# Kernel optimization log

Hardware: AMD Instinct MI355X
Metric: run time of the kernel (lower is better)

## Reference

```python
import jax, jax.numpy as jnp
import numpy as np

N_NODES = 100000
N_EDGES = 1600000
DIM = 3
HID = 128
BN_EPS = 1e-5


def _bn(x, g, b):
    # BatchNorm1d, training-mode batch statistics (biased variance, like torch)
    m = jnp.mean(x, axis=0)
    v = jnp.var(x, axis=0)
    return (x - m) * jax.lax.rsqrt(v + BN_EPS) * g + b


def _gin_mlp(h, w1, b1, g1, be1, w2, b2, g2, be2, w3, b3):
    # Linear -> BN -> ReLU -> (Dropout: identity in eval) -> Linear -> BN -> ReLU -> Linear
    h = jax.nn.relu(_bn(h @ w1 + b1, g1, be1))
    h = jax.nn.relu(_bn(h @ w2 + b2, g2, be2))
    return h @ w3 + b3


def _gin_conv(x, src, dst, eps, mlp_params):
    # GINConv: mlp((1+eps)*x_i + sum_{j->i} x_j); scatter-add over edge targets
    agg = jax.ops.segment_sum(x[src], dst, num_segments=N_NODES)
    return _gin_mlp((1.0 + eps) * x + agg, *mlp_params)


def setup_inputs() -> dict:
    key = jax.random.key(0)
    ks = jax.random.split(key, 32)

    def w(k, shape, scale=0.05):
        return jax.random.normal(k, shape, dtype=jnp.float32) * scale

    inp = {}
    inp["coords"] = jax.random.normal(ks[0], (N_NODES, DIM), dtype=jnp.float32)
    inp["edge_index"] = jax.random.randint(ks[1], (2, N_EDGES), 0, N_NODES, dtype=jnp.int32)

    # GIN layer 0 MLP (dim -> hid -> hid -> hid)
    inp["g0_w1"] = w(ks[2], (DIM, HID)); inp["g0_b1"] = jnp.zeros((HID,), jnp.float32)
    inp["g0_g1"] = jnp.ones((HID,), jnp.float32); inp["g0_be1"] = jnp.zeros((HID,), jnp.float32)
    inp["g0_w2"] = w(ks[3], (HID, HID)); inp["g0_b2"] = jnp.zeros((HID,), jnp.float32)
    inp["g0_g2"] = jnp.ones((HID,), jnp.float32); inp["g0_be2"] = jnp.zeros((HID,), jnp.float32)
    inp["g0_w3"] = w(ks[4], (HID, HID)); inp["g0_b3"] = jnp.zeros((HID,), jnp.float32)
    inp["eps0"] = jnp.zeros((), jnp.float32)
    inp["bn0_g"] = jnp.ones((HID,), jnp.float32); inp["bn0_b"] = jnp.zeros((HID,), jnp.float32)

    # GIN layer 1 MLP (hid -> hid -> hid -> hid)
    inp["g1_w1"] = w(ks[5], (HID, HID)); inp["g1_b1"] = jnp.zeros((HID,), jnp.float32)
    inp["g1_g1"] = jnp.ones((HID,), jnp.float32); inp["g1_be1"] = jnp.zeros((HID,), jnp.float32)
    inp["g1_w2"] = w(ks[6], (HID, HID)); inp["g1_b2"] = jnp.zeros((HID,), jnp.float32)
    inp["g1_g2"] = jnp.ones((HID,), jnp.float32); inp["g1_be2"] = jnp.zeros((HID,), jnp.float32)
    inp["g1_w3"] = w(ks[7], (HID, HID)); inp["g1_b3"] = jnp.zeros((HID,), jnp.float32)
    inp["eps1"] = jnp.zeros((), jnp.float32)
    inp["bn1_g"] = jnp.ones((HID,), jnp.float32); inp["bn1_b"] = jnp.zeros((HID,), jnp.float32)

    # decoder MLP: (2*hid+1) -> hid -> hid//2 -> 1, sigmoid
    inp["d_w1"] = w(ks[8], (2 * HID + 1, HID)); inp["d_b1"] = jnp.zeros((HID,), jnp.float32)
    inp["d_g"] = jnp.ones((HID,), jnp.float32); inp["d_be"] = jnp.zeros((HID,), jnp.float32)
    inp["d_w2"] = w(ks[9], (HID, HID // 2)); inp["d_b2"] = jnp.zeros((HID // 2,), jnp.float32)
    inp["d_w3"] = w(ks[10], (HID // 2, 1)); inp["d_b3"] = jnp.zeros((1,), jnp.float32)
    return inp


def reference(coords, edge_index,
              g0_w1, g0_b1, g0_g1, g0_be1, g0_w2, g0_b2, g0_g2, g0_be2, g0_w3, g0_b3, eps0, bn0_g, bn0_b,
              g1_w1, g1_b1, g1_g1, g1_be1, g1_w2, g1_b2, g1_g2, g1_be2, g1_w3, g1_b3, eps1, bn1_g, bn1_b,
              d_w1, d_b1, d_g, d_be, d_w2, d_b2, d_w3, d_b3):
    node_0 = edge_index[0]
    node_1 = edge_index[1]

    mlp0 = (g0_w1, g0_b1, g0_g1, g0_be1, g0_w2, g0_b2, g0_g2, g0_be2, g0_w3, g0_b3)
    mlp1 = (g1_w1, g1_b1, g1_g1, g1_be1, g1_w2, g1_b2, g1_g2, g1_be2, g1_w3, g1_b3)

    x = _gin_conv(coords, node_0, node_1, eps0, mlp0)
    x = jax.nn.relu(_bn(x, bn0_g, bn0_b))
    x = _gin_conv(x, node_0, node_1, eps1, mlp1)
    x = jax.nn.relu(_bn(x, bn1_g, bn1_b))

    # edge_l_cntr branch: per-edge contour-length feature + endpoint concat
    l = jnp.linalg.norm(coords[node_1] - coords[node_0], axis=1, keepdims=True)  # [E,1]
    h = jnp.concatenate([x[node_0], x[node_1], l], axis=-1)  # [E, 2*hid+1]

    h = jax.nn.relu(_bn(h @ d_w1 + d_b1, d_g, d_be))
    h = jax.nn.relu(h @ d_w2 + d_b2)
    out = jax.nn.sigmoid((h @ d_w3 + d_b3).squeeze(-1))  # [E]
    return out
```

## Files before the change

### kernel.cpp

```cpp
#include <hip/hip_runtime.h>
#include <hip/hip_bf16.h>
#include <math.h>


typedef __attribute__((ext_vector_type(8))) __bf16 bf16x8;
typedef __attribute__((ext_vector_type(4))) float f32x4;

__device__ __forceinline__ unsigned int pack_bf16(float a, float b) {
    unsigned short ua = __builtin_bit_cast(unsigned short, __float2bfloat16(a));
    unsigned short ub = __builtin_bit_cast(unsigned short, __float2bfloat16(b));
    return (unsigned int)ua | ((unsigned int)ub << 16);
}
__device__ __forceinline__ float bflo(unsigned int u) {
    return __builtin_bit_cast(float, u << 16);
}
__device__ __forceinline__ float bfhi(unsigned int u) {
    return __builtin_bit_cast(float, u & 0xffff0000u);
}
__device__ __forceinline__ unsigned short bf16r(float a) {
    return __builtin_bit_cast(unsigned short, __float2bfloat16(a));
}


__global__ void hist_dst(const int* __restrict__ edst, int* __restrict__ cursor, int E) {
    int e = blockIdx.x * 256 + threadIdx.x;
    if (e < E) atomicAdd(&cursor[edst[e]], 1);
}

__global__ __launch_bounds__(1024) void scan_deg(const int* deg, int* rowoff, int* cursor, int N) {
    __shared__ int sums[1024];
    const int t = threadIdx.x;
    const int chunk = (N + 1023) >> 10;
    int lo = t * chunk, hi = lo + chunk;
    if (lo > N) lo = N;
    if (hi > N) hi = N;
    int s = 0;
    for (int i = lo; i < hi; ++i) s += deg[i];
    sums[t] = s;
    __syncthreads();
    for (int off = 1; off < 1024; off <<= 1) {
        int add = (t >= off) ? sums[t - off] : 0;
        __syncthreads();
        sums[t] += add;
        __syncthreads();
    }
    int run = sums[t] - s;
    for (int i = lo; i < hi; ++i) {
        int d = deg[i];
        rowoff[i] = run;
        cursor[i] = run;
        run += d;
    }
    if (t == 1023) rowoff[N] = sums[1023];
}

__global__ void fill_csr(const int* __restrict__ esrc, const int* __restrict__ edst,
                         const float* __restrict__ coords,
                         int* cursor, int* __restrict__ perm, int* __restrict__ dperm,
                         int* __restrict__ eperm, float* __restrict__ lperm, int E) {
    int e = blockIdx.x * 256 + threadIdx.x;
    if (e >= E) return;
    int s0 = esrc[e], d0 = edst[e];
    int pos = atomicAdd(&cursor[d0], 1);
    perm[pos] = s0;
    dperm[pos] = d0;
    eperm[pos] = e;
    float dx = coords[d0*3+0] - coords[s0*3+0];
    float dy = coords[d0*3+1] - coords[s0*3+1];
    float dz = coords[d0*3+2] - coords[s0*3+2];
    lperm[pos] = sqrtf(dx*dx + dy*dy + dz*dz);
}


__global__ void gather_coords(const float* __restrict__ coords,
                              const int* __restrict__ rowoff, const int* __restrict__ perm,
                              float* __restrict__ agg0, int N) {
    int i = blockIdx.x * 256 + threadIdx.x;
    if (i >= N) return;
    float ax = 0.f, ay = 0.f, az = 0.f;
    int b = rowoff[i], t = rowoff[i+1];
    for (int j = b; j < t; ++j) {
        int p = perm[j];
        ax += coords[p*3+0];
        ay += coords[p*3+1];
        az += coords[p*3+2];
    }
    agg0[i*3+0] = ax; agg0[i*3+1] = ay; agg0[i*3+2] = az;
}

__global__ __launch_bounds__(256) void gather_combine_bn(const unsigned short* __restrict__ x,
                                                         const int* __restrict__ rowoff,
                                                         const int* __restrict__ perm,
                                                         const float* __restrict__ st,
                                                         const float* __restrict__ g,
                                                         const float* __restrict__ be,
                                                         float invN,
                                                         const float* __restrict__ eps,
                                                         unsigned short* __restrict__ y, int N) {
    int node = blockIdx.x * 4 + (threadIdx.x >> 6);
    int lane = threadIdx.x & 63;
    if (node >= N) return;
    float ep = 1.f + *eps;
    int c0 = lane*2, c1 = c0 + 1;
    float m0 = st[c0]*invN, m1 = st[c1]*invN;
    float v0 = fmaxf(st[128+c0]*invN - m0*m0, 0.f);
    float v1 = fmaxf(st[128+c1]*invN - m1*m1, 0.f);
    float a0 = g[c0]*rsqrtf(v0 + 1e-5f), a1 = g[c1]*rsqrtf(v1 + 1e-5f);
    float sx = a0, sy = a1;
    float hx = be[c0] - m0*a0, hy = be[c1] - m1*a1;
    const unsigned int* x2 = (const unsigned int*)x;
    int b = rowoff[node], t = rowoff[node+1];
    float accx = 0.f, accy = 0.f;
    int j = b;
    for (; j + 2 <= t; j += 2) {
        unsigned int u0 = x2[(size_t)perm[j]*64 + lane];
        unsigned int u1 = x2[(size_t)perm[j+1]*64 + lane];
        accx += fmaxf(fmaf(bflo(u0), sx, hx), 0.f) + fmaxf(fmaf(bflo(u1), sx, hx), 0.f);
        accy += fmaxf(fmaf(bfhi(u0), sy, hy), 0.f) + fmaxf(fmaf(bfhi(u1), sy, hy), 0.f);
    }
    if (j < t) {
        unsigned int u = x2[(size_t)perm[j]*64 + lane];
        accx += fmaxf(fmaf(bflo(u), sx, hx), 0.f);
        accy += fmaxf(fmaf(bfhi(u), sy, hy), 0.f);
    }
    unsigned int uo = x2[(size_t)node*64 + lane];
    accx = fmaf(ep, fmaxf(fmaf(bflo(uo), sx, hx), 0.f), accx);
    accy = fmaf(ep, fmaxf(fmaf(bfhi(uo), sy, hy), 0.f), accy);
    ((unsigned int*)y)[(size_t)node*64 + lane] = pack_bf16(accx, accy);
}


__global__ __launch_bounds__(256) void lin0(const float* __restrict__ coords,
                                            const float* __restrict__ agg0,
                                            const float* __restrict__ W1,
                                            const float* __restrict__ b1,
                                            const float* __restrict__ eps0,
                                            unsigned short* __restrict__ t1,
                                            float* __restrict__ stats, int nrows) {
    int col = threadIdx.x & 127, half = threadIdx.x >> 7;
    float w0 = W1[col], w1 = W1[128+col], w2 = W1[256+col], bb = b1[col];
    float ep = 1.f + *eps0;
    float s = 0.f, q = 0.f;
    int r0 = blockIdx.x * 64;
    for (int i = 0; i < 32; ++i) {
        int row = r0 + half + 2*i;
        if (row < nrows) {
            float h0 = fmaf(ep, coords[row*3+0], agg0[row*3+0]);
            float h1 = fmaf(ep, coords[row*3+1], agg0[row*3+1]);
            float h2 = fmaf(ep, coords[row*3+2], agg0[row*3+2]);
            float v = fmaf(h0, w0, fmaf(h1, w1, fmaf(h2, w2, bb)));
            t1[row*128+col] = bf16r(v);
            s += v; q += v*v;
        }
    }
    __shared__ float red[512];
    red[half*128+col] = s;
    red[256 + half*128+col] = q;
    __syncthreads();
    if (threadIdx.x < 128) {
        atomicAdd(&stats[col],       red[col] + red[128+col]);
        atomicAdd(&stats[128+col],   red[256+col] + red[384+col]);
    }
}

__global__ void prep_w2(const float* __restrict__ W2, unsigned short* __restrict__ w2t) {
    int i = blockIdx.x * 256 + threadIdx.x;
    if (i >= 128*64) return;
    int k = i >> 6, c = i & 63;
    w2t[c*128 + k] = bf16r(W2[i]);
}

__global__ void prep_wT(const float* __restrict__ w0, const float* __restrict__ w1,
                        const float* __restrict__ w2, const float* __restrict__ w3,
                        const float* __restrict__ w4, const float* __restrict__ w5,
                        const float* __restrict__ w6, unsigned short* __restrict__ dst) {
    int m = blockIdx.y;
    const float* src = (m==0)?w0:(m==1)?w1:(m==2)?w2:(m==3)?w3:(m==4)?w4:(m==5)?w5:w6;
    int i = blockIdx.x * 256 + threadIdx.x;
    int k = i >> 7, c = i & 127;
    dst[m*16384 + c*128 + k] = bf16r(src[i]);
}

template<bool IN_BN, bool STATS>
__global__ __launch_bounds__(256) void gemm_mfma(const unsigned short* __restrict__ A,
                                                 const unsigned short* __restrict__ wT,
                                                 const float* __restrict__ bias,
                                                 const float* __restrict__ inst,
                                                 const float* __restrict__ bng,
                                                 const float* __restrict__ bnb,
                                                 float invCnt,
                                                 unsigned short* __restrict__ Cb,
                                                 float* __restrict__ stats, int nrows) {
    __shared__ int4 sAi[1024];
    __shared__ int4 sBi[2048];
    __shared__ float sred[2][4][128];
    char* sA = (char*)sAi;
    char* sB = (char*)sBi;
    float* sSC = &sred[0][0][0];
    float* sSH = &sred[0][1][0];
    const int tid = threadIdx.x;
    const int tile0 = blockIdx.x * 64;

    if (IN_BN) {
        if (tid < 128) {
            float m = inst[tid] * invCnt;
            float v = fmaxf(inst[128+tid] * invCnt - m*m, 0.f);
            float a = bng[tid] * rsqrtf(v + 1e-5f);
            sSC[tid] = a;
            sSH[tid] = bnb[tid] - m*a;
        }
        __syncthreads();
    }

    {
        const int4* src = (const int4*)wT;
        #pragma unroll
        for (int ii = 0; ii < 8; ++ii) {
            int s = tid + 256*ii;
            int col = s >> 4, k16 = s & 15;
            int byte = ((col << 8) + (k16 << 4)) ^ ((col & 7) << 4);
            *(int4*)(sB + byte) = src[s];
        }
    }
    {
        const int4* A4 = (const int4*)A;
        #pragma unroll
        for (int ii = 0; ii < 4; ++ii) {
            int s = tid + 256*ii;
            int r = s >> 4, k16 = s & 15;
            int row = tile0 + r;
            int4 raw = make_int4(0,0,0,0);
            if (row < nrows) raw = A4[(size_t)row*16 + k16];
            if (IN_BN) {
                float4 sa = ((const float4*)sSC)[k16*2];
                float4 sb = ((const float4*)sSC)[k16*2+1];
                float4 ha = ((const float4*)sSH)[k16*2];
                float4 hb = ((const float4*)sSH)[k16*2+1];
                unsigned int ux = raw.x, uy = raw.y, uz = raw.z, uw = raw.w;
                float e0 = fmaxf(fmaf(bflo(ux), sa.x, ha.x), 0.f);
                float e1 = fmaxf(fmaf(bfhi(ux), sa.y, ha.y), 0.f);
                float e2 = fmaxf(fmaf(bflo(uy), sa.z, ha.z), 0.f);
                float e3 = fmaxf(fmaf(bfhi(uy), sa.w, ha.w), 0.f);
                float e4 = fmaxf(fmaf(bflo(uz), sb.x, hb.x), 0.f);
                float e5 = fmaxf(fmaf(bfhi(uz), sb.y, hb.y), 0.f);
                float e6 = fmaxf(fmaf(bflo(uw), sb.z, hb.z), 0.f);
                float e7 = fmaxf(fmaf(bfhi(uw), sb.w, hb.w), 0.f);
                raw.x = (int)pack_bf16(e0, e1);
                raw.y = (int)pack_bf16(e2, e3);
                raw.z = (int)pack_bf16(e4, e5);
                raw.w = (int)pack_bf16(e6, e7);
            }
            int byte = ((r << 8) + (k16 << 4)) ^ ((r & 7) << 4);
            *(int4*)(sA + byte) = raw;
        }
    }
    __syncthreads();

    const int l = tid & 63;
    const int w = tid >> 6;
    const int arow = (w << 4) + (l & 15);
    const int kbase = (l >> 4) << 3;
    f32x4 accv[8];
    #pragma unroll
    for (int c = 0; c < 8; ++c) accv[c] = (f32x4){0.f, 0.f, 0.f, 0.f};

    #pragma unroll
    for (int t = 0; t < 4; ++t) {
        int k0 = t*32 + kbase;
        int abyte = ((arow << 8) + (k0 << 1)) ^ ((arow & 7) << 4);
        bf16x8 af = __builtin_bit_cast(bf16x8, *(const int4*)(sA + abyte));
        #pragma unroll
        for (int c = 0; c < 8; ++c) {
            int bcol = (c << 4) + (l & 15);
            int bbyte = ((bcol << 8) + (k0 << 1)) ^ ((bcol & 7) << 4);
            bf16x8 bf = __builtin_bit_cast(bf16x8, *(const int4*)(sB + bbyte));
            accv[c] = __builtin_amdgcn_mfma_f32_16x16x32_bf16(af, bf, accv[c], 0, 0, 0);
        }
    }

    const int rj = (l >> 4) << 2;
    float lsum[8], lsq[8];
    #pragma unroll
    for (int c = 0; c < 8; ++c) {
        int col = (c << 4) + (l & 15);
        float bv = bias ? bias[col] : 0.f;
        f32x4 a = accv[c];
        float s = 0.f, q = 0.f;
        #pragma unroll
        for (int j = 0; j < 4; ++j) {
            int row = tile0 + (w << 4) + rj + j;
            float o = a[j] + bv;
            if (row < nrows) {
                Cb[(size_t)row*128 + col] = bf16r(o);
                if (STATS) { s += o; q += o*o; }
            }
        }
        lsum[c] = s; lsq[c] = q;
    }
    if (STATS) {
        #pragma unroll
        for (int c = 0; c < 8; ++c) {
            lsum[c] += __shfl_xor(lsum[c], 16, 64);
            lsum[c] += __shfl_xor(lsum[c], 32, 64);
            lsq[c]  += __shfl_xor(lsq[c], 16, 64);
            lsq[c]  += __shfl_xor(lsq[c], 32, 64);
        }
        __syncthreads();
        if ((l >> 4) == 0) {
            #pragma unroll
            for (int c = 0; c < 8; ++c) {
                int col = (c << 4) + l;
                sred[0][w][col] = lsum[c];
                sred[1][w][col] = lsq[c];
            }
        }
        __syncthreads();
        if (tid < 128) {
            float s = sred[0][0][tid] + sred[0][1][tid] + sred[0][2][tid] + sred[0][3][tid];
            float q = sred[1][0][tid] + sred[1][1][tid] + sred[1][2][tid] + sred[1][3][tid];
            atomicAdd(&stats[tid], s);
            atomicAdd(&stats[128 + tid], q);
        }
    }
}

__global__ __launch_bounds__(256) void csr_stats(const unsigned short* __restrict__ ya,
                                                 const unsigned short* __restrict__ yb,
                                                 const int* __restrict__ rowoff,
                                                 const int* __restrict__ perm,
                                                 const float* __restrict__ lperm,
                                                 const float* __restrict__ wl,
                                                 const float* __restrict__ b1,
                                                 float* __restrict__ stats, int N, int nspan) {
    int w = blockIdx.x * 4 + (threadIdx.x >> 6);
    int lane = threadIdx.x & 63;
    const unsigned int* ya2 = (const unsigned int*)ya;
    const unsigned int* yb2 = (const unsigned int*)yb;
    float2 wl2 = ((const float2*)wl)[lane];
    float2 b12 = ((const float2*)b1)[lane];
    float2 s = make_float2(0.f, 0.f), q = make_float2(0.f, 0.f);
    int i0 = w * nspan;
    int i1 = i0 + nspan; if (i1 > N) i1 = N;
    for (int i = i0; i < i1; ++i) {
        unsigned int ub = yb2[(size_t)i*64 + lane];
        float ybx = bflo(ub), yby = bfhi(ub);
        int b = rowoff[i], t = rowoff[i+1];
        for (int j = b; j < t; ++j) {
            int p = perm[j];
            float lv = lperm[j];
            unsigned int ua = ya2[(size_t)p*64 + lane];
            float zx = bflo(ua) + ybx + fmaf(lv, wl2.x, b12.x);
            float zy = bfhi(ua) + yby + fmaf(lv, wl2.y, b12.y);
            s.x += zx; s.y += zy;
            q.x += zx*zx; q.y += zy*zy;
        }
    }
    __shared__ float red[1024];
    int wv = threadIdx.x >> 6;
    red[wv*128 + lane*2]       = s.x;
    red[wv*128 + lane*2 + 1]   = s.y;
    red[512 + wv*128 + lane*2]     = q.x;
    red[512 + wv*128 + lane*2 + 1] = q.y;
    __syncthreads();
    if (threadIdx.x < 128) {
        int c = threadIdx.x;
        float ss = red[c] + red[128+c] + red[256+c] + red[384+c];
        float qq = red[512+c] + red[640+c] + red[768+c] + red[896+c];
        atomicAdd(&stats[c], ss);
        atomicAdd(&stats[128+c], qq);
    }
}

__global__ __launch_bounds__(256) void decoder_fused(const unsigned short* __restrict__ ya,
                                                     const unsigned short* __restrict__ yb,
                                                     const float* __restrict__ lperm,
                                                     const int* __restrict__ perm,
                                                     const int* __restrict__ dperm,
                                                     const int* __restrict__ eperm,
                                                     const float* __restrict__ wl,
                                                     const float* __restrict__ b1,
                                                     const float* __restrict__ st6,
                                                     const float* __restrict__ dg,
                                                     const float* __restrict__ dbe,
                                                     float invE,
                                                     const unsigned short* __restrict__ w2t,
                                                     const float* __restrict__ b2,
                                                     const float* __restrict__ w3,
                                                     const float* __restrict__ b3p,
                                                     float* __restrict__ out, int E, int ntiles) {
    __shared__ int4 sAB[2048];
    char* sA = (char*)sAB;
    char* sB = (char*)sAB + 16384;
    const int tid = threadIdx.x;

    {
        const int4* src = (const int4*)w2t;
        #pragma unroll
        for (int ii = 0; ii < 4; ++ii) {
            int s = tid + 256*ii;
            int col = s >> 4, k16 = s & 15;
            int byte = ((col << 8) + (k16 << 4)) ^ ((col & 7) << 4);
            *(int4*)(sB + byte) = src[s];
        }
    }

    const int c4 = tid & 31;
    const int rb = tid >> 5;
    float4 wv = ((const float4*)wl)[c4];
    float4 bb = ((const float4*)b1)[c4];
    float4 s4, t4;
    {
        int cb = c4 * 4;
        #pragma unroll
        for (int j = 0; j < 4; ++j) {
            float m = st6[cb+j] * invE;
            float v = fmaxf(st6[128+cb+j] * invE - m*m, 0.f);
            float a = dg[cb+j] * rsqrtf(v + 1e-5f);
            ((float*)&s4)[j] = a;
            ((float*)&t4)[j] = dbe[cb+j] - m*a;
        }
    }
    const uint2* ya2 = (const uint2*)ya;
    const uint2* yb2 = (const uint2*)yb;

    const int l = tid & 63;
    const int w = tid >> 6;
    const int arow = (w << 4) + (l & 15);
    const int kbase = (l >> 4) << 3;
    const float b3v = b3p[0];

    for (int tile = blockIdx.x; tile < ntiles; tile += gridDim.x) {
        const int tile0 = tile * 64;
        __syncthreads();
        #pragma unroll
        for (int i = 0; i < 8; ++i) {
            int r = rb + 8*i;
            int row = tile0 + r;
            float4 v = make_float4(0.f, 0.f, 0.f, 0.f);
            if (row < E) {
                int s0 = perm[row], d0 = dperm[row];
                float lv = lperm[row];
                uint2 ua = ya2[(size_t)s0*32 + c4];
                uint2 ubv = yb2[(size_t)d0*32 + c4];
                float vax = bflo(ua.x), vay = bfhi(ua.x), vaz = bflo(ua.y), vaw = bfhi(ua.y);
                float vbx = bflo(ubv.x), vby = bfhi(ubv.x), vbz = bflo(ubv.y), vbw = bfhi(ubv.y);
                v.x = fmaxf(fmaf(vax + vbx + fmaf(lv, wv.x, bb.x), s4.x, t4.x), 0.f);
                v.y = fmaxf(fmaf(vay + vby + fmaf(lv, wv.y, bb.y), s4.y, t4.y), 0.f);
                v.z = fmaxf(fmaf(vaz + vbz + fmaf(lv, wv.z, bb.z), s4.z, t4.z), 0.f);
                v.w = fmaxf(fmaf(vaw + vbw + fmaf(lv, wv.w, bb.w), s4.w, t4.w), 0.f);
            }
            uint2 pk;
            pk.x = pack_bf16(v.x, v.y);
            pk.y = pack_bf16(v.z, v.w);
            int byte = ((r << 8) + (c4 << 3)) ^ ((r & 7) << 4);
            *(uint2*)(sA + byte) = pk;
        }
        __syncthreads();

        f32x4 accv[4];
        #pragma unroll
        for (int c = 0; c < 4; ++c) accv[c] = (f32x4){0.f, 0.f, 0.f, 0.f};
        #pragma unroll
        for (int t = 0; t < 4; ++t) {
            int k0 = t*32 + kbase;
            int abyte = ((arow << 8) + (k0 << 1)) ^ ((arow & 7) << 4);
            bf16x8 af = __builtin_bit_cast(bf16x8, *(const int4*)(sA + abyte));
            #pragma unroll
            for (int c = 0; c < 4; ++c) {
                int bcol = (c << 4) + (l & 15);
                int bbyte = ((bcol << 8) + (k0 << 1)) ^ ((bcol & 7) << 4);
                bf16x8 bf = __builtin_bit_cast(bf16x8, *(const int4*)(sB + bbyte));
                accv[c] = __builtin_amdgcn_mfma_f32_16x16x32_bf16(af, bf, accv[c], 0, 0, 0);
            }
        }

        float p0 = 0.f, p1 = 0.f, p2 = 0.f, p3 = 0.f;
        #pragma unroll
        for (int c = 0; c < 4; ++c) {
            int col = (c << 4) + (l & 15);
            float b2c = b2[col], w3c = w3[col];
            f32x4 a = accv[c];
            p0 = fmaf(fmaxf(a[0] + b2c, 0.f), w3c, p0);
            p1 = fmaf(fmaxf(a[1] + b2c, 0.f), w3c, p1);
            p2 = fmaf(fmaxf(a[2] + b2c, 0.f), w3c, p2);
            p3 = fmaf(fmaxf(a[3] + b2c, 0.f), w3c, p3);
        }
        #pragma unroll
        for (int m = 1; m < 16; m <<= 1) {
            p0 += __shfl_xor(p0, m, 64);
            p1 += __shfl_xor(p1, m, 64);
            p2 += __shfl_xor(p2, m, 64);
            p3 += __shfl_xor(p3, m, 64);
        }
        if ((l & 15) == 0) {
            int rbase = tile0 + (w << 4) + ((l >> 4) << 2);
            float pj[4] = {p0, p1, p2, p3};
            #pragma unroll
            for (int j = 0; j < 4; ++j) {
                int row = rbase + j;
                if (row < E) out[eperm[row]] = 1.f / (1.f + expf(-(pj[j] + b3v)));
            }
        }
    }
}


extern "C" void kernel_launch(void* const* d_in, const int* in_sizes, int n_in,
                              void* d_out, int out_size, void* d_ws, size_t ws_size,
                              hipStream_t stream) {
    const int N = in_sizes[0] / 3;
    const int E = in_sizes[1] / 2;

    const float* coords = (const float*)d_in[0];
    const int*   ei     = (const int*)d_in[1];
    const int*   esrc = ei;
    const int*   edst = ei + E;
    const float* g0_w1 = (const float*)d_in[2];
    const float* g0_b1 = (const float*)d_in[3];
    const float* g0_g1 = (const float*)d_in[4];
    const float* g0_be1= (const float*)d_in[5];
    const float* g0_w2 = (const float*)d_in[6];
    const float* g0_b2 = (const float*)d_in[7];
    const float* g0_g2 = (const float*)d_in[8];
    const float* g0_be2= (const float*)d_in[9];
    const float* g0_w3 = (const float*)d_in[10];
    const float* g0_b3 = (const float*)d_in[11];
    const float* eps0  = (const float*)d_in[12];
    const float* bn0_g = (const float*)d_in[13];
    const float* bn0_b = (const float*)d_in[14];
    const float* g1_w1 = (const float*)d_in[15];
    const float* g1_b1 = (const float*)d_in[16];
    const float* g1_g1 = (const float*)d_in[17];
    const float* g1_be1= (const float*)d_in[18];
    const float* g1_w2 = (const float*)d_in[19];
    const float* g1_b2 = (const float*)d_in[20];
    const float* g1_g2 = (const float*)d_in[21];
    const float* g1_be2= (const float*)d_in[22];
    const float* g1_w3 = (const float*)d_in[23];
    const float* g1_b3 = (const float*)d_in[24];
    const float* eps1  = (const float*)d_in[25];
    const float* bn1_g = (const float*)d_in[26];
    const float* bn1_b = (const float*)d_in[27];
    const float* d_w1  = (const float*)d_in[28];
    const float* d_b1  = (const float*)d_in[29];
    const float* d_g   = (const float*)d_in[30];
    const float* d_be  = (const float*)d_in[31];
    const float* d_w2  = (const float*)d_in[32];
    const float* d_b2  = (const float*)d_in[33];
    const float* d_w3  = (const float*)d_in[34];
    const float* d_b3  = (const float*)d_in[35];

    float* ws = (float*)d_ws;
    const size_t NF = (size_t)N * 128;
    float* buf0 = ws;
    float* buf1 = ws + NF;
    float* buf2 = ws + 2*NF;
    float* agg0 = ws + 3*NF;
    float* stats= agg0 + (size_t)N*3;
    float* scsh = stats + 7*256;
    float* lperm = scsh + 7*256;
    int*   cursor = (int*)(lperm + E);
    int*   rowoff = cursor + N;
    int*   perm   = rowoff + N + 1;
    int*   dperm  = perm + E;
    int*   eperm  = dperm + E;
    unsigned short* w2t = (unsigned short*)(eperm + E);
    unsigned short* wT  = w2t + 64*128;

    unsigned short* b0 = (unsigned short*)buf0;
    unsigned short* b1b = (unsigned short*)buf1;
    unsigned short* b2b = (unsigned short*)buf2;

    float* out = (float*)d_out;

    const float* wl = d_w1 + 256*128;

    #define STATSK(k) (stats + (k)*256)
    #define WT(m) (wT + (m)*16384)

    const int rowTiles = (N + 63) / 64;
    const int edgeTiles = (E + 63) / 64;
    const int eBlocks = (E + 255) / 256;
    const float invN = 1.f / (float)N;
    const float invE = 1.f / (float)E;
    const int nWaves = 2048 * 4;
    const int nspan = (N + nWaves - 1) / nWaves;
    const int decBlocks = 1280;

    hipMemsetAsync(stats, 0, 7*256 * sizeof(float), stream);
    hipMemsetAsync(cursor, 0, (size_t)N * sizeof(int), stream);

    hist_dst<<<eBlocks, 256, 0, stream>>>(edst, cursor, E);
    scan_deg<<<1, 1024, 0, stream>>>(cursor, rowoff, cursor, N);
    fill_csr<<<eBlocks, 256, 0, stream>>>(esrc, edst, coords, cursor, perm, dperm, eperm, lperm, E);
    prep_w2<<<32, 256, 0, stream>>>(d_w2, w2t);
    prep_wT<<<dim3(64, 7), 256, 0, stream>>>(g0_w2, g0_w3, g1_w1, g1_w2, g1_w3,
                                             d_w1, d_w1 + 128*128, wT);

    gather_coords<<<(N + 255)/256, 256, 0, stream>>>(coords, rowoff, perm, agg0, N);
    lin0<<<rowTiles, 256, 0, stream>>>(coords, agg0, g0_w1, g0_b1, eps0, b0, STATSK(0), N);
    gemm_mfma<true,true><<<rowTiles, 256, 0, stream>>>(
        b0, WT(0), g0_b2, STATSK(0), g0_g1, g0_be1, invN, b1b, STATSK(1), N);
    gemm_mfma<true,true><<<rowTiles, 256, 0, stream>>>(
        b1b, WT(1), g0_b3, STATSK(1), g0_g2, g0_be2, invN, b2b, STATSK(2), N);

    gather_combine_bn<<<(N + 3)/4, 256, 0, stream>>>(
        b2b, rowoff, perm, STATSK(2), bn0_g, bn0_b, invN, eps1, b0, N);
    gemm_mfma<false,true><<<rowTiles, 256, 0, stream>>>(
        b0, WT(2), g1_b1, nullptr, nullptr, nullptr, 0.f, b1b, STATSK(3), N);
    gemm_mfma<true,true><<<rowTiles, 256, 0, stream>>>(
        b1b, WT(3), g1_b2, STATSK(3), g1_g1, g1_be1, invN, b2b, STATSK(4), N);
    gemm_mfma<true,true><<<rowTiles, 256, 0, stream>>>(
        b2b, WT(4), g1_b3, STATSK(4), g1_g2, g1_be2, invN, b0, STATSK(5), N);

    gemm_mfma<true,false><<<rowTiles, 256, 0, stream>>>(
        b0, WT(5), nullptr, STATSK(5), bn1_g, bn1_b, invN, b1b, nullptr, N);
    gemm_mfma<true,false><<<rowTiles, 256, 0, stream>>>(
        b0, WT(6), nullptr, STATSK(5), bn1_g, bn1_b, invN, b2b, nullptr, N);
    csr_stats<<<2048, 256, 0, stream>>>(b1b, b2b, rowoff, perm, lperm, wl, d_b1,
                                        STATSK(6), N, nspan);
    decoder_fused<<<decBlocks, 256, 0, stream>>>(b1b, b2b, lperm, perm, dperm, eperm,
                                                 wl, d_b1, STATSK(6), d_g, d_be, invE,
                                                 w2t, d_b2, d_w3, d_b3, out, E, edgeTiles);
}
```

Before: 1.500 ms.

## Hold decoder W2 in registers, launch one block per edge tile, unroll csr_stats

The decoder kernel no longer copies the W2 tile into shared memory or loops persistently over tiles. Each wave now loads its B fragments for the MFMA straight from global memory into registers, and the launch uses one block per 64-edge tile, which halves LDS use and removes a per-tile barrier. The csr_stats inner loop is unrolled by two to issue more independent gathers. In exchange, every block reloads W2 from global/L2 (25k blocks), and the larger register footprint may lower occupancy.

```diff
diff --git a/kernel.cpp b/kernel.cpp
--- a/kernel.cpp
+++ b/kernel.cpp
@@ -345,7 +345,21 @@
         unsigned int ub = yb2[(size_t)i*64 + lane];
         float ybx = bflo(ub), yby = bfhi(ub);
         int b = rowoff[i], t = rowoff[i+1];
-        for (int j = b; j < t; ++j) {
+        int j = b;
+        for (; j + 2 <= t; j += 2) {
+            int p0 = perm[j], p1 = perm[j+1];
+            float l0 = lperm[j], l1 = lperm[j+1];
+            unsigned int ua0 = ya2[(size_t)p0*64 + lane];
+            unsigned int ua1 = ya2[(size_t)p1*64 + lane];
+            float z0x = bflo(ua0) + ybx + fmaf(l0, wl2.x, b12.x);
+            float z0y = bfhi(ua0) + yby + fmaf(l0, wl2.y, b12.y);
+            float z1x = bflo(ua1) + ybx + fmaf(l1, wl2.x, b12.x);
+            float z1y = bfhi(ua1) + yby + fmaf(l1, wl2.y, b12.y);
+            s.x += z0x + z1x; s.y += z0y + z1y;
+            q.x += fmaf(z0x, z0x, z1x*z1x);
+            q.y += fmaf(z0y, z0y, z1y*z1y);
+        }
+        if (j < t) {
             int p = perm[j];
             float lv = lperm[j];
             unsigned int ua = ya2[(size_t)p*64 + lane];
@@ -387,51 +401,48 @@
                                                      const float* __restrict__ b2,
                                                      const float* __restrict__ w3,
                                                      const float* __restrict__ b3p,
-                                                     float* __restrict__ out, int E, int ntiles) {
-    __shared__ int4 sAB[2048];
-    char* sA = (char*)sAB;
-    char* sB = (char*)sAB + 16384;
+                                                     float* __restrict__ out, int E) {
+    __shared__ int4 sAi[1024];
+    char* sA = (char*)sAi;
     const int tid = threadIdx.x;
-
-    {
-        const int4* src = (const int4*)w2t;
-        #pragma unroll
-        for (int ii = 0; ii < 4; ++ii) {
-            int s = tid + 256*ii;
-            int col = s >> 4, k16 = s & 15;
-            int byte = ((col << 8) + (k16 << 4)) ^ ((col & 7) << 4);
-            *(int4*)(sB + byte) = src[s];
-        }
-    }
-
-    const int c4 = tid & 31;
-    const int rb = tid >> 5;
-    float4 wv = ((const float4*)wl)[c4];
-    float4 bb = ((const float4*)b1)[c4];
-    float4 s4, t4;
-    {
-        int cb = c4 * 4;
-        #pragma unroll
-        for (int j = 0; j < 4; ++j) {
-            float m = st6[cb+j] * invE;
-            float v = fmaxf(st6[128+cb+j] * invE - m*m, 0.f);
-            float a = dg[cb+j] * rsqrtf(v + 1e-5f);
-            ((float*)&s4)[j] = a;
-            ((float*)&t4)[j] = dbe[cb+j] - m*a;
-        }
-    }
-    const uint2* ya2 = (const uint2*)ya;
-    const uint2* yb2 = (const uint2*)yb;
-
+    const int tile0 = blockIdx.x * 64;
     const int l = tid & 63;
     const int w = tid >> 6;
-    const int arow = (w << 4) + (l & 15);
-    const int kbase = (l >> 4) << 3;
-    const float b3v = b3p[0];
-
-    for (int tile = blockIdx.x; tile < ntiles; tile += gridDim.x) {
-        const int tile0 = tile * 64;
-        __syncthreads();
+
+    bf16x8 breg[4][4];
+    {
+        const int colidx = l & 15;
+        const int krow = (l >> 4) << 3;
+        #pragma unroll
+        for (int t = 0; t < 4; ++t)
+            #pragma unroll
+            for (int c = 0; c < 4; ++c) {
+                int bcol = (c << 4) + colidx;
+                int k0 = t*32 + krow;
+                breg[t][c] = __builtin_bit_cast(bf16x8,
+                    *(const int4*)(w2t + bcol*128 + k0));
+            }
+    }
+
+    {
+        const int c4 = tid & 31;
+        const int rb = tid >> 5;
+        float4 wv = ((const float4*)wl)[c4];
+        float4 bb = ((const float4*)b1)[c4];
+        float4 s4, t4;
+        {
+            int cb = c4 * 4;
+            #pragma unroll
+            for (int j = 0; j < 4; ++j) {
+                float m = st6[cb+j] * invE;
+                float v = fmaxf(st6[128+cb+j] * invE - m*m, 0.f);
+                float a = dg[cb+j] * rsqrtf(v + 1e-5f);
+                ((float*)&s4)[j] = a;
+                ((float*)&t4)[j] = dbe[cb+j] - m*a;
+            }
+        }
+        const uint2* ya2 = (const uint2*)ya;
+        const uint2* yb2 = (const uint2*)yb;
         #pragma unroll
         for (int i = 0; i < 8; ++i) {
             int r = rb + 8*i;
@@ -455,51 +466,52 @@
             int byte = ((r << 8) + (c4 << 3)) ^ ((r & 7) << 4);
             *(uint2*)(sA + byte) = pk;
         }
-        __syncthreads();
-
-        f32x4 accv[4];
-        #pragma unroll
-        for (int c = 0; c < 4; ++c) accv[c] = (f32x4){0.f, 0.f, 0.f, 0.f};
-        #pragma unroll
-        for (int t = 0; t < 4; ++t) {
-            int k0 = t*32 + kbase;
-            int abyte = ((arow << 8) + (k0 << 1)) ^ ((arow & 7) << 4);
-            bf16x8 af = __builtin_bit_cast(bf16x8, *(const int4*)(sA + abyte));
-            #pragma unroll
-            for (int c = 0; c < 4; ++c) {
-                int bcol = (c << 4) + (l & 15);
-                int bbyte = ((bcol << 8) + (k0 << 1)) ^ ((bcol & 7) << 4);
-                bf16x8 bf = __builtin_bit_cast(bf16x8, *(const int4*)(sB + bbyte));
-                accv[c] = __builtin_amdgcn_mfma_f32_16x16x32_bf16(af, bf, accv[c], 0, 0, 0);
-            }
-        }
-
-        float p0 = 0.f, p1 = 0.f, p2 = 0.f, p3 = 0.f;
+    }
+    __syncthreads();
+
+    const int arow = (w << 4) + (l & 15);
+    const int kbase = (l >> 4) << 3;
+    f32x4 accv[4];
+    #pragma unroll
+    for (int c = 0; c < 4; ++c) accv[c] = (f32x4){0.f, 0.f, 0.f, 0.f};
+
+    #pragma unroll
+    for (int t = 0; t < 4; ++t) {
+        int k0 = t*32 + kbase;
+        int abyte = ((arow << 8) + (k0 << 1)) ^ ((arow & 7) << 4);
+        bf16x8 af = __builtin_bit_cast(bf16x8, *(const int4*)(sA + abyte));
         #pragma unroll
         for (int c = 0; c < 4; ++c) {
-            int col = (c << 4) + (l & 15);
-            float b2c = b2[col], w3c = w3[col];
-            f32x4 a = accv[c];
-            p0 = fmaf(fmaxf(a[0] + b2c, 0.f), w3c, p0);
-            p1 = fmaf(fmaxf(a[1] + b2c, 0.f), w3c, p1);
-            p2 = fmaf(fmaxf(a[2] + b2c, 0.f), w3c, p2);
-            p3 = fmaf(fmaxf(a[3] + b2c, 0.f), w3c, p3);
-        }
-        #pragma unroll
-        for (int m = 1; m < 16; m <<= 1) {
-            p0 += __shfl_xor(p0, m, 64);
-            p1 += __shfl_xor(p1, m, 64);
-            p2 += __shfl_xor(p2, m, 64);
-            p3 += __shfl_xor(p3, m, 64);
-        }
-        if ((l & 15) == 0) {
-            int rbase = tile0 + (w << 4) + ((l >> 4) << 2);
-            float pj[4] = {p0, p1, p2, p3};
-            #pragma unroll
-            for (int j = 0; j < 4; ++j) {
-                int row = rbase + j;
-                if (row < E) out[eperm[row]] = 1.f / (1.f + expf(-(pj[j] + b3v)));
-            }
+            accv[c] = __builtin_amdgcn_mfma_f32_16x16x32_bf16(af, breg[t][c], accv[c], 0, 0, 0);
+        }
+    }
+
+    float p0 = 0.f, p1 = 0.f, p2 = 0.f, p3 = 0.f;
+    #pragma unroll
+    for (int c = 0; c < 4; ++c) {
+        int col = (c << 4) + (l & 15);
+        float b2c = b2[col], w3c = w3[col];
+        f32x4 a = accv[c];
+        p0 = fmaf(fmaxf(a[0] + b2c, 0.f), w3c, p0);
+        p1 = fmaf(fmaxf(a[1] + b2c, 0.f), w3c, p1);
+        p2 = fmaf(fmaxf(a[2] + b2c, 0.f), w3c, p2);
+        p3 = fmaf(fmaxf(a[3] + b2c, 0.f), w3c, p3);
+    }
+    #pragma unroll
+    for (int m = 1; m < 16; m <<= 1) {
+        p0 += __shfl_xor(p0, m, 64);
+        p1 += __shfl_xor(p1, m, 64);
+        p2 += __shfl_xor(p2, m, 64);
+        p3 += __shfl_xor(p3, m, 64);
+    }
+    if ((l & 15) == 0) {
+        float b3v = b3p[0];
+        int rbase = tile0 + (w << 4) + ((l >> 4) << 2);
+        float pj[4] = {p0, p1, p2, p3};
+        #pragma unroll
+        for (int j = 0; j < 4; ++j) {
+            int row = rbase + j;
+            if (row < E) out[eperm[row]] = 1.f / (1.f + expf(-(pj[j] + b3v)));
         }
     }
 }
@@ -585,7 +597,6 @@
     const float invE = 1.f / (float)E;
     const int nWaves = 2048 * 4;
     const int nspan = (N + nWaves - 1) / nWaves;
-    const int decBlocks = 1280;
 
     hipMemsetAsync(stats, 0, 7*256 * sizeof(float), stream);
     hipMemsetAsync(cursor, 0, (size_t)N * sizeof(int), stream);
@@ -619,7 +630,7 @@
         b0, WT(6), nullptr, STATSK(5), bn1_g, bn1_b, invN, b2b, nullptr, N);
     csr_stats<<<2048, 256, 0, stream>>>(b1b, b2b, rowoff, perm, lperm, wl, d_b1,
                                         STATSK(6), N, nspan);
-    decoder_fused<<<decBlocks, 256, 0, stream>>>(b1b, b2b, lperm, perm, dperm, eperm,
+    decoder_fused<<<edgeTiles, 256, 0, stream>>>(b1b, b2b, lperm, perm, dperm, eperm,
                                                  wl, d_b1, STATSK(6), d_g, d_be, invE,
-                                                 w2t, d_b2, d_w3, d_b3, out, E, edgeTiles);
-}
+                                                 w2t, d_b2, d_w3, d_b3, out, E);
+}
```

Measured after the change: 1.573 ms. 1.05x slower.
